# Performance work log

Measured on AMD Instinct MI355X. Metric: run time of the kernel, lower is better.

## Reference

```python
import jax, jax.numpy as jnp
import numpy as np
from itertools import permutations

B = 16384      # batch size
M = 6          # number of DOA sources (M! = 720 permutations)
PERMS = np.array(list(permutations(range(M))), dtype=np.int32)  # [720, M]


def setup_inputs() -> dict:
    key = jax.random.key(0)
    k1, k2 = jax.random.split(key)
    doa_predictions = jax.random.uniform(k1, (B, M), dtype=jnp.float32)
    doa = jax.random.uniform(k2, (B, M), dtype=jnp.float32)
    return {"doa_predictions": doa_predictions, "doa": doa}


def reference(doa_predictions, doa):
    perms = jnp.asarray(PERMS)                      # [P, M] static permutation indices
    pp = doa_predictions[:, perms]                  # [B, P, M] all permuted predictions
    half_pi = jnp.float32(np.pi / 2)
    pi = jnp.float32(np.pi)
    # periodic error wrapped into [-pi/2, pi/2)
    err = jnp.mod(pp - doa[:, None, :] + half_pi, pi) - half_pi
    # RMSPE per permutation: ||err|| / sqrt(M)
    rmspe = jnp.sqrt(jnp.sum(err * err, axis=-1)) * jnp.float32(1.0 / np.sqrt(M))  # [B, P]
    return jnp.sum(jnp.min(rmspe, axis=1))          # sum over batch of per-sample best alignment
```

## Files before the change

kernel.cpp:

```cpp
#include <hip/hip_runtime.h>
#include <math.h>

#define NB 16384
#define M 6
#define GRID 64
#define BLOCK 256

__global__ __launch_bounds__(BLOCK) void rmspe_fused(const float* __restrict__ pred,
                                                     const float* __restrict__ doa,
                                                     float* __restrict__ partial,
                                                     unsigned int* __restrict__ flags,
                                                     float* __restrict__ out) {
    const int b = blockIdx.x * BLOCK + threadIdx.x;

    float p[M], d[M];
    const float2* pv = reinterpret_cast<const float2*>(pred + (size_t)b * M);
    const float2* dv = reinterpret_cast<const float2*>(doa  + (size_t)b * M);
    #pragma unroll
    for (int i = 0; i < 3; ++i) {
        float2 a = pv[i]; p[2*i] = a.x; p[2*i+1] = a.y;
        float2 c = dv[i]; d[2*i] = c.x; d[2*i+1] = c.y;
    }

    const float HALF_PI = 1.57079632679489661923f;
    const float PI      = 3.14159265358979323846f;
    const float INV_PI  = 0.31830988618379067154f;

    float e2[M][M];
    #pragma unroll
    for (int i = 0; i < M; ++i) {
        #pragma unroll
        for (int j = 0; j < M; ++j) {
            float x = p[j] - d[i] + HALF_PI;
            float m = x - PI * floorf(x * INV_PI);
            float e = m - HALF_PI;
            e2[i][j] = e * e;
        }
    }

    float f[64];
    f[0] = 0.0f;
    #pragma unroll
    for (int S = 1; S < 64; ++S) {
        const int k = __builtin_popcount(S) - 1;
        float best = 0.0f;
        bool first = true;
        #pragma unroll
        for (int j = 0; j < M; ++j) {
            if (!(S & (1 << j))) continue;
            const float cand = f[S ^ (1 << j)] + e2[k][j];
            best = first ? cand : fminf(best, cand);
            first = false;
        }
        f[S] = best;
    }

    float v = sqrtf(f[63]) * 0.40824829046386301637f;

    #pragma unroll
    for (int off = 32; off > 0; off >>= 1)
        v += __shfl_down(v, off, 64);

    __shared__ float wsum[4];
    const int lane = threadIdx.x & 63;
    const int wid  = threadIdx.x >> 6;
    if (lane == 0) wsum[wid] = v;
    __syncthreads();

    if (threadIdx.x == 0) {
        const float bs = (wsum[0] + wsum[1]) + (wsum[2] + wsum[3]);
        __hip_atomic_store(&partial[blockIdx.x], bs,
                           __ATOMIC_RELAXED, __HIP_MEMORY_SCOPE_AGENT);
        __hip_atomic_store(&flags[blockIdx.x], 1u,
                           __ATOMIC_RELEASE, __HIP_MEMORY_SCOPE_AGENT);
    }

    if (blockIdx.x == 0 && wid == 0) {
        unsigned int fl;
        do {
            fl = __hip_atomic_load(&flags[lane],
                                   __ATOMIC_ACQUIRE, __HIP_MEMORY_SCOPE_AGENT);
        } while (!__all(fl == 1u));
        float s = __hip_atomic_load(&partial[lane],
                                    __ATOMIC_RELAXED, __HIP_MEMORY_SCOPE_AGENT);
        #pragma unroll
        for (int off = 32; off > 0; off >>= 1)
            s += __shfl_down(s, off, 64);
        if (lane == 0) out[0] = s;
    }
}

extern "C" void kernel_launch(void* const* d_in, const int* in_sizes, int n_in,
                              void* d_out, int out_size, void* d_ws, size_t ws_size,
                              hipStream_t stream) {
    const float* pred = (const float*)d_in[0];
    const float* doa  = (const float*)d_in[1];
    float* partial       = (float*)d_ws;
    unsigned int* flags  = (unsigned int*)((char*)d_ws + 256);
    float* out = (float*)d_out;

    rmspe_fused<<<GRID, BLOCK, 0, stream>>>(pred, doa, partial, flags, out);
}
```

Before: 9.948 us.

## Use 256 single-wave blocks with packed flag/value slots and dedicated reducer block

Replaces 64 blocks of 256 threads with 256 one-wave compute blocks plus a dedicated reducer block 0. Each compute block publishes its partial sum and ready flag in a single 64-bit release store, and the reducer polls 256 slots. This spreads the work across more CUs and removes the LDS/__syncthreads intra-block reduction. The costs are a larger spin poll, and the approach relies on the reducer block co-residing with the compute blocks.

```diff
diff --git a/kernel.cpp b/kernel.cpp
--- a/kernel.cpp
+++ b/kernel.cpp
@@ -3,15 +3,40 @@
 
 #define NB 16384
 #define M 6
-#define GRID 64
-#define BLOCK 256
+#define CBLOCKS 256
+#define GRID (CBLOCKS + 1)
 
-__global__ __launch_bounds__(BLOCK) void rmspe_fused(const float* __restrict__ pred,
-                                                     const float* __restrict__ doa,
-                                                     float* __restrict__ partial,
-                                                     unsigned int* __restrict__ flags,
-                                                     float* __restrict__ out) {
-    const int b = blockIdx.x * BLOCK + threadIdx.x;
+__global__ __launch_bounds__(64) void rmspe_fused(const float* __restrict__ pred,
+                                                  const float* __restrict__ doa,
+                                                  unsigned long long* __restrict__ slots,
+                                                  float* __restrict__ out) {
+    const int lane = threadIdx.x;
+
+    if (blockIdx.x == 0) {
+        unsigned long long v[4];
+        bool ok;
+        do {
+            ok = true;
+            #pragma unroll
+            for (int k = 0; k < 4; ++k) {
+                v[k] = __hip_atomic_load(&slots[lane * 4 + k],
+                                         __ATOMIC_ACQUIRE, __HIP_MEMORY_SCOPE_AGENT);
+                ok = ok && ((unsigned int)v[k] == 1u);
+            }
+        } while (!__all(ok));
+
+        float s = 0.0f;
+        #pragma unroll
+        for (int k = 0; k < 4; ++k)
+            s += __uint_as_float((unsigned int)(v[k] >> 32));
+        #pragma unroll
+        for (int off = 32; off > 0; off >>= 1)
+            s += __shfl_down(s, off, 64);
+        if (lane == 0) out[0] = s;
+        return;
+    }
+
+    const int b = (blockIdx.x - 1) * 64 + lane;
 
     float p[M], d[M];
     const float2* pv = reinterpret_cast<const float2*>(pred + (size_t)b * M);
@@ -61,32 +86,11 @@
     for (int off = 32; off > 0; off >>= 1)
         v += __shfl_down(v, off, 64);
 
-    __shared__ float wsum[4];
-    const int lane = threadIdx.x & 63;
-    const int wid  = threadIdx.x >> 6;
-    if (lane == 0) wsum[wid] = v;
-    __syncthreads();
-
-    if (threadIdx.x == 0) {
-        const float bs = (wsum[0] + wsum[1]) + (wsum[2] + wsum[3]);
-        __hip_atomic_store(&partial[blockIdx.x], bs,
-                           __ATOMIC_RELAXED, __HIP_MEMORY_SCOPE_AGENT);
-        __hip_atomic_store(&flags[blockIdx.x], 1u,
+    if (lane == 0) {
+        const unsigned long long pk =
+            ((unsigned long long)__float_as_uint(v) << 32) | 1ull;
+        __hip_atomic_store(&slots[blockIdx.x - 1], pk,
                            __ATOMIC_RELEASE, __HIP_MEMORY_SCOPE_AGENT);
-    }
-
-    if (blockIdx.x == 0 && wid == 0) {
-        unsigned int fl;
-        do {
-            fl = __hip_atomic_load(&flags[lane],
-                                   __ATOMIC_ACQUIRE, __HIP_MEMORY_SCOPE_AGENT);
-        } while (!__all(fl == 1u));
-        float s = __hip_atomic_load(&partial[lane],
-                                    __ATOMIC_RELAXED, __HIP_MEMORY_SCOPE_AGENT);
-        #pragma unroll
-        for (int off = 32; off > 0; off >>= 1)
-            s += __shfl_down(s, off, 64);
-        if (lane == 0) out[0] = s;
     }
 }
 
@@ -95,9 +99,8 @@
                               hipStream_t stream) {
     const float* pred = (const float*)d_in[0];
     const float* doa  = (const float*)d_in[1];
-    float* partial       = (float*)d_ws;
-    unsigned int* flags  = (unsigned int*)((char*)d_ws + 256);
+    unsigned long long* slots = (unsigned long long*)d_ws;
     float* out = (float*)d_out;
 
-    rmspe_fused<<<GRID, BLOCK, 0, stream>>>(pred, doa, partial, flags, out);
+    rmspe_fused<<<GRID, 64, 0, stream>>>(pred, doa, slots, out);
 }
```

New measurement: 11.02 us. 1.11x slower.
